# Optimization experiments

Measured on AMD Instinct MI355X. Metric: run time of the kernel, lower is better.

The kernel has to match this reference:

```python
import jax, jax.numpy as jnp
import numpy as np


def setup_inputs() -> dict:
    key = jax.random.key(0)
    k1, k2, k3 = jax.random.split(key, 3)
    B, M, J = 4096, 64, 24  # batch, n_max_markers, n_joints
    points = jax.random.normal(k1, (B, M, 3), dtype=jnp.float32)
    weight = jax.random.uniform(k2, (B, M, J), dtype=jnp.float32)  # positive soft weights
    offset = jax.random.normal(k3, (B, M, J, 3), dtype=jnp.float32)
    return {"points": points, "weight": weight, "offset": offset}


def reference(points, weight, offset):
    # P: per-joint marker offsets (B, J, 3, M); Q: world marker positions (B, 1, 3, M)
    P = jnp.transpose(offset, (0, 2, 3, 1))
    Q = jnp.transpose(points, (0, 2, 1))[:, None]
    w = jnp.transpose(weight, (0, 2, 1))[:, :, None]  # (B, J, 1, M)

    wsum = jnp.sum(w, axis=-1)                   # (B, J, 1)
    P_ = jnp.sum(P * w, axis=-1) / wsum          # (B, J, 3) weighted centroid of offsets
    Q_ = jnp.sum(Q * w, axis=-1) / wsum          # (B, J, 3) weighted centroid of markers

    X = P - P_[..., None]                        # (B, J, 3, M)
    Y = Q - Q_[..., None]                        # (B, J, 3, M) via broadcast

    # Cross-covariance S = X @ Y^T (NOTE: original multiplies un-weighted centered coords)
    S = jnp.einsum('bjdm,bjem->bjde', X, Y)      # (B, J, 3, 3)

    U, _, Vh = jnp.linalg.svd(S)
    V = jnp.swapaxes(Vh, -1, -2)
    Ut = jnp.swapaxes(U, -1, -2)
    det = jnp.linalg.det(jnp.matmul(V, Ut))      # (B, J) reflection correction
    Ut = Ut.at[..., -1, :].multiply(det[..., None])
    R = jnp.matmul(V, Ut)                        # (B, J, 3, 3) optimal rotation
    t = Q_[..., None] - jnp.matmul(R, P_[..., None])  # (B, J, 3, 1)
    return R, t
```

## Files before the change

### kernel.cpp

```cpp
#include <hip/hip_runtime.h>


constexpr int M = 64;
constexpr int J = 24;
constexpr int NACC = 22;
constexpr int NWS  = 15;
constexpr int BPG  = 4;

constexpr int L4_W = 0;
constexpr int L4_O = 384;
constexpr int L4_P = 1536;
constexpr int L4_N = 1584;

template<int P, int Q>
__device__ __forceinline__ void jrot(float A[4][4], float V[4][4]) {
    float apq = A[P][Q];
    float theta = (A[Q][Q] - A[P][P]) * __builtin_amdgcn_rcpf(2.0f * apq);
    float t = __builtin_amdgcn_rcpf(fabsf(theta) + __builtin_amdgcn_sqrtf(fmaf(theta, theta, 1.0f)));
    t = (theta < 0.0f) ? -t : t;
    t = (apq == 0.0f) ? 0.0f : t;
    float c = __builtin_amdgcn_rsqf(fmaf(t, t, 1.0f));
    float s = t * c;
#pragma unroll
    for (int k = 0; k < 4; ++k) {
        float akp = A[k][P], akq = A[k][Q];
        A[k][P] = c * akp - s * akq;
        A[k][Q] = s * akp + c * akq;
    }
#pragma unroll
    for (int k = 0; k < 4; ++k) {
        float apk = A[P][k], aqk = A[Q][k];
        A[P][k] = c * apk - s * aqk;
        A[Q][k] = s * apk + c * aqk;
        float vkp = V[k][P], vkq = V[k][Q];
        V[k][P] = c * vkp - s * vkq;
        V[k][Q] = s * vkp + c * vkq;
    }
}

__device__ __forceinline__ void horn_solve(
    float S00, float S01, float S02, float S10, float S11, float S12,
    float S20, float S21, float S22,
    float cP0, float cP1, float cP2, float cQ0, float cQ1, float cQ2,
    float* __restrict__ Rout, float* __restrict__ tout)
{
    float A[4][4], V[4][4];
    A[0][0] = S00 + S11 + S22;
    A[0][1] = A[1][0] = S12 - S21;
    A[0][2] = A[2][0] = S20 - S02;
    A[0][3] = A[3][0] = S01 - S10;
    A[1][1] = S00 - S11 - S22;
    A[1][2] = A[2][1] = S01 + S10;
    A[1][3] = A[3][1] = S02 + S20;
    A[2][2] = -S00 + S11 - S22;
    A[2][3] = A[3][2] = S12 + S21;
    A[3][3] = -S00 - S11 + S22;
#pragma unroll
    for (int r = 0; r < 4; ++r)
#pragma unroll
        for (int c = 0; c < 4; ++c)
            V[r][c] = (r == c) ? 1.0f : 0.0f;

#pragma unroll 1
    for (int sweep = 0; sweep < 6; ++sweep) {
        jrot<0, 1>(A, V); jrot<0, 2>(A, V); jrot<0, 3>(A, V);
        jrot<1, 2>(A, V); jrot<1, 3>(A, V); jrot<2, 3>(A, V);
    }

    float best = A[0][0];
    float qw = V[0][0], qx = V[1][0], qy = V[2][0], qz = V[3][0];
#pragma unroll
    for (int i = 1; i < 4; ++i) {
        bool better = A[i][i] > best;
        best = better ? A[i][i] : best;
        qw = better ? V[0][i] : qw;
        qx = better ? V[1][i] : qx;
        qy = better ? V[2][i] : qy;
        qz = better ? V[3][i] : qz;
    }
    float nrm = __builtin_amdgcn_rsqf(qw * qw + qx * qx + qy * qy + qz * qz);
    qw *= nrm; qx *= nrm; qy *= nrm; qz *= nrm;

    float R00 = 1.f - 2.f * (qy * qy + qz * qz);
    float R01 = 2.f * (qx * qy - qw * qz);
    float R02 = 2.f * (qx * qz + qw * qy);
    float R10 = 2.f * (qx * qy + qw * qz);
    float R11 = 1.f - 2.f * (qx * qx + qz * qz);
    float R12 = 2.f * (qy * qz - qw * qx);
    float R20 = 2.f * (qx * qz - qw * qy);
    float R21 = 2.f * (qy * qz + qw * qx);
    float R22 = 1.f - 2.f * (qx * qx + qy * qy);

    Rout[0] = R00; Rout[1] = R01; Rout[2] = R02;
    Rout[3] = R10; Rout[4] = R11; Rout[5] = R12;
    Rout[6] = R20; Rout[7] = R21; Rout[8] = R22;
    tout[0] = cQ0 - (R00 * cP0 + R01 * cP1 + R02 * cP2);
    tout[1] = cQ1 - (R10 * cP0 + R11 * cP1 + R12 * cP2);
    tout[2] = cQ2 - (R20 * cP0 + R21 * cP1 + R22 * cP2);
}

__global__ __launch_bounds__(256, 4) void kabsch_fused(
    const float* __restrict__ points,
    const float* __restrict__ weight,
    const float* __restrict__ offset,
    float* __restrict__ out,
    int B, int bj_total)
{
    const int b0 = blockIdx.x * BPG;
    const int t  = threadIdx.x;

    __shared__ float4 lds4[L4_N];
    __shared__ float  sv_s[BPG][NWS][J + 1];

    const int lane = t & 63;
    const int wv   = t >> 6;
    const int kk   = lane & 7;
    const int jj   = (lane >> 3) + wv * 8;
    const bool prod = (jj < J);

    float4 r_o0, r_o1, r_o2, r_o3, r_o4, r_w0, r_w1, r_p0;
    auto load_batch = [&](int bb) {
        bb = bb < B ? bb : B - 1;
        const float4* wb4 = (const float4*)(weight + (size_t)bb * (M * J));
        const float4* ob4 = (const float4*)(offset + (size_t)bb * (M * J * 3));
        const float4* pb4 = (const float4*)(points + (size_t)bb * (M * 3));
        r_o0 = ob4[t];
        r_o1 = ob4[t + 256];
        r_o2 = ob4[t + 512];
        r_o3 = ob4[t + 768];
        r_w0 = wb4[t];
        if (t < 128) { r_o4 = ob4[1024 + t]; r_w1 = wb4[256 + t]; }
        if (t < 48)  { r_p0 = pb4[t]; }
    };

    load_batch(b0);

#pragma unroll 1
    for (int g = 0; g < BPG; ++g) {
        lds4[L4_O + t]       = r_o0;
        lds4[L4_O + 256 + t] = r_o1;
        lds4[L4_O + 512 + t] = r_o2;
        lds4[L4_O + 768 + t] = r_o3;
        lds4[L4_W + t]       = r_w0;
        if (t < 128) { lds4[L4_O + 1024 + t] = r_o4; lds4[L4_W + 256 + t] = r_w1; }
        if (t < 48)  { lds4[L4_P + t] = r_p0; }

        __syncthreads();

        if (g + 1 < BPG) load_batch(b0 + g + 1);

        float acc[NACC];
#pragma unroll
        for (int n = 0; n < NACC; ++n) acc[n] = 0.0f;

        if (prod) {
            const float* w_s = (const float*)lds4;
            const float* o_s = (const float*)lds4 + 4 * L4_O;
            const float* p_s = (const float*)lds4 + 4 * L4_P;

#pragma unroll
            for (int i = 0; i < M / 8; ++i) {
                const int m = i * 8 + kk;
                float w  = w_s[m * J + jj];
                float o0 = o_s[m * 72 + jj * 3 + 0];
                float o1 = o_s[m * 72 + jj * 3 + 1];
                float o2 = o_s[m * 72 + jj * 3 + 2];
                float p0 = p_s[m * 3 + 0];
                float p1 = p_s[m * 3 + 1];
                float p2 = p_s[m * 3 + 2];
                acc[0] += w;
                acc[1] = fmaf(w, o0, acc[1]);  acc[2] = fmaf(w, o1, acc[2]);  acc[3] = fmaf(w, o2, acc[3]);
                acc[4] = fmaf(w, p0, acc[4]);  acc[5] = fmaf(w, p1, acc[5]);  acc[6] = fmaf(w, p2, acc[6]);
                acc[7] += o0; acc[8] += o1; acc[9] += o2;
                acc[10] += p0; acc[11] += p1; acc[12] += p2;
                acc[13] = fmaf(o0, p0, acc[13]); acc[14] = fmaf(o0, p1, acc[14]); acc[15] = fmaf(o0, p2, acc[15]);
                acc[16] = fmaf(o1, p0, acc[16]); acc[17] = fmaf(o1, p1, acc[17]); acc[18] = fmaf(o1, p2, acc[18]);
                acc[19] = fmaf(o2, p0, acc[19]); acc[20] = fmaf(o2, p1, acc[20]); acc[21] = fmaf(o2, p2, acc[21]);
            }

#pragma unroll
            for (int n = 0; n < NACC; ++n) {
                float v = acc[n];
                v += __shfl_xor(v, 1);
                v += __shfl_xor(v, 2);
                v += __shfl_xor(v, 4);
                acc[n] = v;
            }

            if (kk == 0) {
                const float inv = __builtin_amdgcn_rcpf(acc[0]);
                const float cP0 = acc[1] * inv, cP1 = acc[2] * inv, cP2 = acc[3] * inv;
                const float cQ0 = acc[4] * inv, cQ1 = acc[5] * inv, cQ2 = acc[6] * inv;
                const float To0 = acc[7], To1 = acc[8], To2 = acc[9];
                const float Tp0 = acc[10], Tp1 = acc[11], Tp2 = acc[12];
                const float fM = (float)M;
                sv_s[g][0][jj]  = acc[13] - cP0 * Tp0 - cQ0 * To0 + fM * cP0 * cQ0;
                sv_s[g][1][jj]  = acc[14] - cP0 * Tp1 - cQ1 * To0 + fM * cP0 * cQ1;
                sv_s[g][2][jj]  = acc[15] - cP0 * Tp2 - cQ2 * To0 + fM * cP0 * cQ2;
                sv_s[g][3][jj]  = acc[16] - cP1 * Tp0 - cQ0 * To1 + fM * cP1 * cQ0;
                sv_s[g][4][jj]  = acc[17] - cP1 * Tp1 - cQ1 * To1 + fM * cP1 * cQ1;
                sv_s[g][5][jj]  = acc[18] - cP1 * Tp2 - cQ2 * To1 + fM * cP1 * cQ2;
                sv_s[g][6][jj]  = acc[19] - cP2 * Tp0 - cQ0 * To2 + fM * cP2 * cQ0;
                sv_s[g][7][jj]  = acc[20] - cP2 * Tp1 - cQ1 * To2 + fM * cP2 * cQ1;
                sv_s[g][8][jj]  = acc[21] - cP2 * Tp2 - cQ2 * To2 + fM * cP2 * cQ2;
                sv_s[g][9][jj]  = cP0; sv_s[g][10][jj] = cP1; sv_s[g][11][jj] = cP2;
                sv_s[g][12][jj] = cQ0; sv_s[g][13][jj] = cQ1; sv_s[g][14][jj] = cQ2;
            }
        }

        __syncthreads();
    }

    if (t < BPG * J) {
        const int g  = t / J;
        const int j  = t - g * J;
        const int bb = b0 + g;
        if (bb < B) {
            float v[NWS];
#pragma unroll
            for (int n = 0; n < NWS; ++n) v[n] = sv_s[g][n][j];
            float Rr[9], tr[3];
            horn_solve(v[0], v[1], v[2], v[3], v[4], v[5], v[6], v[7], v[8],
                       v[9], v[10], v[11], v[12], v[13], v[14], Rr, tr);
            const int bj = bb * J + j;
            float* Rout = out + (size_t)bj * 9;
#pragma unroll
            for (int n = 0; n < 9; ++n) Rout[n] = Rr[n];
            float* tout = out + (size_t)bj_total * 9 + (size_t)bj * 3;
            tout[0] = tr[0]; tout[1] = tr[1]; tout[2] = tr[2];
        }
    }
}

extern "C" void kernel_launch(void* const* d_in, const int* in_sizes, int n_in,
                              void* d_out, int out_size, void* d_ws, size_t ws_size,
                              hipStream_t stream) {
    const float* points = (const float*)d_in[0];
    const float* weight = (const float*)d_in[1];
    const float* offset = (const float*)d_in[2];
    float* out = (float*)d_out;

    int B = in_sizes[0] / (M * 3);
    int bj_total = B * J;
    int grid = (B + BPG - 1) / BPG;

    kabsch_fused<<<grid, 256, 0, stream>>>(points, weight, offset, out, B, bj_total);
}
```

Before: 142.5 us.

## Drop LDS staging: one wave per batch reads global memory directly

Replaces the block-of-4-batches design, which staged weight/offset/points through LDS with register prefetch, with one wave per batch element. Each lane pair handles one joint and reads its 32 markers straight from global memory. The 8-way shuffle reduction becomes a 1-step xor, and the grid grows to B/2 blocks of 128 threads. This removes LDS traffic and the per-iteration barriers, at the cost of strided, poorly coalesced global loads (stride J and 3J floats per lane) and 16 of 64 lanes idle.

```diff
diff --git a/kernel.cpp b/kernel.cpp
--- a/kernel.cpp
+++ b/kernel.cpp
@@ -5,12 +5,7 @@
 constexpr int J = 24;
 constexpr int NACC = 22;
 constexpr int NWS  = 15;
-constexpr int BPG  = 4;
-
-constexpr int L4_W = 0;
-constexpr int L4_O = 384;
-constexpr int L4_P = 1536;
-constexpr int L4_N = 1584;
+constexpr int WPB  = 2;
 
 template<int P, int Q>
 __device__ __forceinline__ void jrot(float A[4][4], float V[4][4]) {
@@ -99,122 +94,82 @@
     tout[2] = cQ2 - (R20 * cP0 + R21 * cP1 + R22 * cP2);
 }
 
-__global__ __launch_bounds__(256, 4) void kabsch_fused(
+__global__ __launch_bounds__(128, 4) void kabsch_fused(
     const float* __restrict__ points,
     const float* __restrict__ weight,
     const float* __restrict__ offset,
     float* __restrict__ out,
     int B, int bj_total)
 {
-    const int b0 = blockIdx.x * BPG;
-    const int t  = threadIdx.x;
-
-    __shared__ float4 lds4[L4_N];
-    __shared__ float  sv_s[BPG][NWS][J + 1];
-
+    const int t    = threadIdx.x;
+    const int wv   = t >> 6;
     const int lane = t & 63;
-    const int wv   = t >> 6;
-    const int kk   = lane & 7;
-    const int jj   = (lane >> 3) + wv * 8;
-    const bool prod = (jj < J);
-
-    float4 r_o0, r_o1, r_o2, r_o3, r_o4, r_w0, r_w1, r_p0;
-    auto load_batch = [&](int bb) {
-        bb = bb < B ? bb : B - 1;
-        const float4* wb4 = (const float4*)(weight + (size_t)bb * (M * J));
-        const float4* ob4 = (const float4*)(offset + (size_t)bb * (M * J * 3));
-        const float4* pb4 = (const float4*)(points + (size_t)bb * (M * 3));
-        r_o0 = ob4[t];
-        r_o1 = ob4[t + 256];
-        r_o2 = ob4[t + 512];
-        r_o3 = ob4[t + 768];
-        r_w0 = wb4[t];
-        if (t < 128) { r_o4 = ob4[1024 + t]; r_w1 = wb4[256 + t]; }
-        if (t < 48)  { r_p0 = pb4[t]; }
-    };
-
-    load_batch(b0);
-
-#pragma unroll 1
-    for (int g = 0; g < BPG; ++g) {
-        lds4[L4_O + t]       = r_o0;
-        lds4[L4_O + 256 + t] = r_o1;
-        lds4[L4_O + 512 + t] = r_o2;
-        lds4[L4_O + 768 + t] = r_o3;
-        lds4[L4_W + t]       = r_w0;
-        if (t < 128) { lds4[L4_O + 1024 + t] = r_o4; lds4[L4_W + 256 + t] = r_w1; }
-        if (t < 48)  { lds4[L4_P + t] = r_p0; }
-
-        __syncthreads();
-
-        if (g + 1 < BPG) load_batch(b0 + g + 1);
+    const int jj   = lane >> 1;
+    const int kk   = lane & 1;
+
+    int bw = blockIdx.x * WPB + wv;
+    bw = bw < B ? bw : B - 1;
+
+    __shared__ float sv_s[WPB][NWS][J + 1];
+
+    if (jj < J) {
+        const float* wq = weight + (size_t)bw * (M * J) + (size_t)(kk * 32) * J + jj;
+        const float* oq = offset + (size_t)bw * (M * J * 3) + (size_t)(kk * 32) * (J * 3) + jj * 3;
+        const float* pq = points + (size_t)bw * (M * 3) + (size_t)(kk * 32) * 3;
 
         float acc[NACC];
 #pragma unroll
         for (int n = 0; n < NACC; ++n) acc[n] = 0.0f;
 
-        if (prod) {
-            const float* w_s = (const float*)lds4;
-            const float* o_s = (const float*)lds4 + 4 * L4_O;
-            const float* p_s = (const float*)lds4 + 4 * L4_P;
-
-#pragma unroll
-            for (int i = 0; i < M / 8; ++i) {
-                const int m = i * 8 + kk;
-                float w  = w_s[m * J + jj];
-                float o0 = o_s[m * 72 + jj * 3 + 0];
-                float o1 = o_s[m * 72 + jj * 3 + 1];
-                float o2 = o_s[m * 72 + jj * 3 + 2];
-                float p0 = p_s[m * 3 + 0];
-                float p1 = p_s[m * 3 + 1];
-                float p2 = p_s[m * 3 + 2];
-                acc[0] += w;
-                acc[1] = fmaf(w, o0, acc[1]);  acc[2] = fmaf(w, o1, acc[2]);  acc[3] = fmaf(w, o2, acc[3]);
-                acc[4] = fmaf(w, p0, acc[4]);  acc[5] = fmaf(w, p1, acc[5]);  acc[6] = fmaf(w, p2, acc[6]);
-                acc[7] += o0; acc[8] += o1; acc[9] += o2;
-                acc[10] += p0; acc[11] += p1; acc[12] += p2;
-                acc[13] = fmaf(o0, p0, acc[13]); acc[14] = fmaf(o0, p1, acc[14]); acc[15] = fmaf(o0, p2, acc[15]);
-                acc[16] = fmaf(o1, p0, acc[16]); acc[17] = fmaf(o1, p1, acc[17]); acc[18] = fmaf(o1, p2, acc[18]);
-                acc[19] = fmaf(o2, p0, acc[19]); acc[20] = fmaf(o2, p1, acc[20]); acc[21] = fmaf(o2, p2, acc[21]);
-            }
-
-#pragma unroll
-            for (int n = 0; n < NACC; ++n) {
-                float v = acc[n];
-                v += __shfl_xor(v, 1);
-                v += __shfl_xor(v, 2);
-                v += __shfl_xor(v, 4);
-                acc[n] = v;
-            }
-
-            if (kk == 0) {
-                const float inv = __builtin_amdgcn_rcpf(acc[0]);
-                const float cP0 = acc[1] * inv, cP1 = acc[2] * inv, cP2 = acc[3] * inv;
-                const float cQ0 = acc[4] * inv, cQ1 = acc[5] * inv, cQ2 = acc[6] * inv;
-                const float To0 = acc[7], To1 = acc[8], To2 = acc[9];
-                const float Tp0 = acc[10], Tp1 = acc[11], Tp2 = acc[12];
-                const float fM = (float)M;
-                sv_s[g][0][jj]  = acc[13] - cP0 * Tp0 - cQ0 * To0 + fM * cP0 * cQ0;
-                sv_s[g][1][jj]  = acc[14] - cP0 * Tp1 - cQ1 * To0 + fM * cP0 * cQ1;
-                sv_s[g][2][jj]  = acc[15] - cP0 * Tp2 - cQ2 * To0 + fM * cP0 * cQ2;
-                sv_s[g][3][jj]  = acc[16] - cP1 * Tp0 - cQ0 * To1 + fM * cP1 * cQ0;
-                sv_s[g][4][jj]  = acc[17] - cP1 * Tp1 - cQ1 * To1 + fM * cP1 * cQ1;
-                sv_s[g][5][jj]  = acc[18] - cP1 * Tp2 - cQ2 * To1 + fM * cP1 * cQ2;
-                sv_s[g][6][jj]  = acc[19] - cP2 * Tp0 - cQ0 * To2 + fM * cP2 * cQ0;
-                sv_s[g][7][jj]  = acc[20] - cP2 * Tp1 - cQ1 * To2 + fM * cP2 * cQ1;
-                sv_s[g][8][jj]  = acc[21] - cP2 * Tp2 - cQ2 * To2 + fM * cP2 * cQ2;
-                sv_s[g][9][jj]  = cP0; sv_s[g][10][jj] = cP1; sv_s[g][11][jj] = cP2;
-                sv_s[g][12][jj] = cQ0; sv_s[g][13][jj] = cQ1; sv_s[g][14][jj] = cQ2;
-            }
+#pragma unroll
+        for (int i = 0; i < M / 2; ++i) {
+            float w  = wq[i * J];
+            float o0 = oq[i * 72 + 0];
+            float o1 = oq[i * 72 + 1];
+            float o2 = oq[i * 72 + 2];
+            float p0 = pq[i * 3 + 0];
+            float p1 = pq[i * 3 + 1];
+            float p2 = pq[i * 3 + 2];
+            acc[0] += w;
+            acc[1] = fmaf(w, o0, acc[1]);  acc[2] = fmaf(w, o1, acc[2]);  acc[3] = fmaf(w, o2, acc[3]);
+            acc[4] = fmaf(w, p0, acc[4]);  acc[5] = fmaf(w, p1, acc[5]);  acc[6] = fmaf(w, p2, acc[6]);
+            acc[7] += o0; acc[8] += o1; acc[9] += o2;
+            acc[10] += p0; acc[11] += p1; acc[12] += p2;
+            acc[13] = fmaf(o0, p0, acc[13]); acc[14] = fmaf(o0, p1, acc[14]); acc[15] = fmaf(o0, p2, acc[15]);
+            acc[16] = fmaf(o1, p0, acc[16]); acc[17] = fmaf(o1, p1, acc[17]); acc[18] = fmaf(o1, p2, acc[18]);
+            acc[19] = fmaf(o2, p0, acc[19]); acc[20] = fmaf(o2, p1, acc[20]); acc[21] = fmaf(o2, p2, acc[21]);
         }
 
-        __syncthreads();
-    }
-
-    if (t < BPG * J) {
+#pragma unroll
+        for (int n = 0; n < NACC; ++n) acc[n] += __shfl_xor(acc[n], 1);
+
+        if (kk == 0) {
+            const float inv = __builtin_amdgcn_rcpf(acc[0]);
+            const float cP0 = acc[1] * inv, cP1 = acc[2] * inv, cP2 = acc[3] * inv;
+            const float cQ0 = acc[4] * inv, cQ1 = acc[5] * inv, cQ2 = acc[6] * inv;
+            const float To0 = acc[7], To1 = acc[8], To2 = acc[9];
+            const float Tp0 = acc[10], Tp1 = acc[11], Tp2 = acc[12];
+            const float fM = (float)M;
+            sv_s[wv][0][jj]  = acc[13] - cP0 * Tp0 - cQ0 * To0 + fM * cP0 * cQ0;
+            sv_s[wv][1][jj]  = acc[14] - cP0 * Tp1 - cQ1 * To0 + fM * cP0 * cQ1;
+            sv_s[wv][2][jj]  = acc[15] - cP0 * Tp2 - cQ2 * To0 + fM * cP0 * cQ2;
+            sv_s[wv][3][jj]  = acc[16] - cP1 * Tp0 - cQ0 * To1 + fM * cP1 * cQ0;
+            sv_s[wv][4][jj]  = acc[17] - cP1 * Tp1 - cQ1 * To1 + fM * cP1 * cQ1;
+            sv_s[wv][5][jj]  = acc[18] - cP1 * Tp2 - cQ2 * To1 + fM * cP1 * cQ2;
+            sv_s[wv][6][jj]  = acc[19] - cP2 * Tp0 - cQ0 * To2 + fM * cP2 * cQ0;
+            sv_s[wv][7][jj]  = acc[20] - cP2 * Tp1 - cQ1 * To2 + fM * cP2 * cQ1;
+            sv_s[wv][8][jj]  = acc[21] - cP2 * Tp2 - cQ2 * To2 + fM * cP2 * cQ2;
+            sv_s[wv][9][jj]  = cP0; sv_s[wv][10][jj] = cP1; sv_s[wv][11][jj] = cP2;
+            sv_s[wv][12][jj] = cQ0; sv_s[wv][13][jj] = cQ1; sv_s[wv][14][jj] = cQ2;
+        }
+    }
+
+    __syncthreads();
+
+    if (t < WPB * J) {
         const int g  = t / J;
         const int j  = t - g * J;
-        const int bb = b0 + g;
+        int bb = blockIdx.x * WPB + g;
         if (bb < B) {
             float v[NWS];
 #pragma unroll
@@ -242,7 +197,7 @@
 
     int B = in_sizes[0] / (M * 3);
     int bj_total = B * J;
-    int grid = (B + BPG - 1) / BPG;
-
-    kabsch_fused<<<grid, 256, 0, stream>>>(points, weight, offset, out, B, bj_total);
-}
+    int grid = (B + WPB - 1) / WPB;
+
+    kabsch_fused<<<grid, 128, 0, stream>>>(points, weight, offset, out, B, bj_total);
+}
```

After: 140.2 us, median of 2. Within noise of the previous version (-1.7%).
